# Kernel optimization log

Hardware: AMD Instinct MI355X
Metric: run time of the kernel (lower is better)

The kernel has to match this reference:

```python
import jax, jax.numpy as jnp
import numpy as np

B, S, D = 64, 8192, 128  # batch, source length, hidden (enc == dec)


def setup_inputs() -> dict:
    key = jax.random.key(0)
    ks = jax.random.split(key, 7)
    s = 1.0 / np.sqrt(D)
    return {
        "input": jax.random.normal(ks[0], (B, D), jnp.float32),
        "context": jax.random.normal(ks[1], (B, S, D), jnp.float32),
        "W_enc": jax.random.uniform(ks[2], (D, D), jnp.float32, -s, s),
        "b_enc": jax.random.uniform(ks[3], (D,), jnp.float32, -s, s),
        "W_dec": jax.random.uniform(ks[4], (D, D), jnp.float32, -s, s),
        "b_dec": jax.random.uniform(ks[5], (D,), jnp.float32, -s, s),
        "W_out": jax.random.uniform(ks[6], (D, 2 * D), jnp.float32, -s, s),  # no bias
    }


def reference(input, context, W_enc, b_enc, W_dec, b_dec, W_out):
    # projected_context = tanh(lin_encoder(context))  [B, S, D]
    pc = jnp.tanh(jnp.einsum("bse,de->bsd", context, W_enc) + b_enc)
    # q = tanh(lin_decoder(input))  [B, D]
    q = jnp.tanh(input @ W_dec.T + b_dec)
    # attention scores via bmm(projected_context, q): [B, S]
    scores = jnp.einsum("bsd,bd->bs", pc, q)
    attn = jax.nn.softmax(scores, axis=1)  # softmax over source positions
    # weighted sum of (raw) context: [B, D]
    weighted_context = jnp.einsum("bs,bsd->bd", attn, context)
    # h_tilde = tanh(linear_out(concat(weighted_context, q)))  [B, D]
    h_tilde = jnp.tanh(jnp.concatenate([weighted_context, q], axis=-1) @ W_out.T)
    return h_tilde, attn
```

## Files before the change

### kernel.cpp

```cpp
#include <hip/hip_runtime.h>
#include <hip/hip_bf16.h>

#define BB 64
#define SS 8192
#define DD 128
#define NCHUNK 8
#define CHROWS 1024
#define NTILE 16

typedef __attribute__((ext_vector_type(8))) short bf16x8;
typedef __attribute__((ext_vector_type(4))) float f32x4;

#define SWZ(c, qd) ((qd) * 16 + ((c) ^ (2 * (qd))))

__device__ __forceinline__ unsigned pk2(float x, float y) {
    __hip_bfloat162 h = __float22bfloat162_rn(make_float2(x, y));
    union { __hip_bfloat162 h2; unsigned u; } cv;
    cv.h2 = h;
    return cv.u;
}

__device__ __forceinline__ float bflo(unsigned p) { return __uint_as_float(p << 16); }
__device__ __forceinline__ float bfhi(unsigned p) { return __uint_as_float(p & 0xffff0000u); }

__device__ __forceinline__ float tanh_fast(float x) {
    float e = __expf(2.f * x);
    return 1.f - 2.f / (e + 1.f);
}

__device__ __forceinline__ void lds_barrier() {
    asm volatile("s_waitcnt lgkmcnt(0)" ::: "memory");
    __builtin_amdgcn_s_barrier();
    asm volatile("" ::: "memory");
}

__global__ void qproj_kernel(const float* __restrict__ input,
                             const float* __restrict__ W_dec,
                             const float* __restrict__ b_dec,
                             float* __restrict__ q) {
    __shared__ float xin[DD];
    const int b = blockIdx.x, d = threadIdx.x;
    xin[d] = input[b * DD + d];
    __syncthreads();
    const float4* wrow = (const float4*)(W_dec + (size_t)d * DD);
    float acc = 0.f;
#pragma unroll
    for (int k4 = 0; k4 < DD / 4; k4++) {
        float4 w = wrow[k4];
        float4 x = ((const float4*)xin)[k4];
        acc += w.x * x.x + w.y * x.y + w.z * x.z + w.w * x.w;
    }
    q[b * DD + d] = tanh_fast(acc + b_dec[d]);
}

#define ISSUE(tile, R) do {                                          \
    const float4* tb_ = base + (size_t)(tile) * 2048;                \
    _Pragma("unroll")                                                \
    for (int i = 0; i < 8; i++) R[i] = tb_[t + 256 * i];             \
} while (0)

#define PACK(buf, R) do {                                            \
    _Pragma("unroll")                                                \
    for (int i = 0; i < 8; i++) {                                    \
        int row_ = rg + 8 * i, w_ = row_ >> 4, c_ = row_ & 15;       \
        int a8_ = (w_ * 4 + ukk) * 128 + SWZ(c_, uqd) * 2 + uh;      \
        uint2 pk_;                                                   \
        pk_.x = pk2(R[i].x, R[i].y);                                 \
        pk_.y = pk2(R[i].z, R[i].w);                                 \
        P[i] = pk_;                                                  \
        *(uint2*)&Cl[buf][a8_ * 4] = pk_;                            \
    }                                                                \
} while (0)

__global__ __launch_bounds__(256, 2) void score_fused_kernel(
    const float* __restrict__ ctx,
    const float* __restrict__ W_enc,
    const float* __restrict__ b_enc,
    const float* __restrict__ q,
    float* __restrict__ scores,
    float* __restrict__ wcp,
    float* __restrict__ Mp,
    float* __restrict__ Tp) {
    __shared__ __align__(16) short Wl[16384];
    __shared__ __align__(16) short Cl[2][8192];
    __shared__ float sw[64];
    __shared__ float4 red[256];

    const int t = threadIdx.x;

    const float4* W4 = (const float4*)W_enc;
    for (int c2 = t; c2 < 2048; c2 += 256) {
        int row = c2 >> 4, kc = c2 & 15;
        float4 f0 = W4[row * 32 + kc * 2];
        float4 f1 = W4[row * 32 + kc * 2 + 1];
        int nt = row >> 4, colw = row & 15, kk = kc >> 2, qd = kc & 3;
        int a8 = (nt * 4 + kk) * 128 + SWZ(colw, qd) * 2;
        uint4 u;
        u.x = pk2(f0.x, f0.y); u.y = pk2(f0.z, f0.w);
        u.z = pk2(f1.x, f1.y); u.w = pk2(f1.z, f1.w);
        *(uint4*)&Wl[a8 * 4] = u;
    }

    const int wv = t >> 6, lane = t & 63;
    const int col = lane & 15, quad = lane >> 4;
    const int b = blockIdx.x >> 3;
    const int chunk = blockIdx.x & 7;

    const int u = t & 31, rg = t >> 5;
    const int ukk = u >> 3, uqd = (u >> 1) & 3, uh = u & 1;

    float qv[8], bv[8];
#pragma unroll
    for (int nt = 0; nt < 8; nt++) {
        qv[nt] = q[b * DD + nt * 16 + col];
        bv[nt] = b_enc[nt * 16 + col];
    }

    const float4* base = (const float4*)(ctx + ((size_t)b * SS + (size_t)chunk * CHROWS) * DD);

    float4 RA[8], RB[8];
    uint2 P[8];

    float Mrun = -INFINITY, Trun = 0.f;
    float4 acc4 = {0.f, 0.f, 0.f, 0.f};

    auto compute_tile = [&](int it, int cur) {
        bf16x8 a[4];
#pragma unroll
        for (int kk = 0; kk < 4; kk++) {
            int a8 = (wv * 4 + kk) * 128 + SWZ(col, quad) * 2;
            a[kk] = *(const bf16x8*)&Cl[cur][a8 * 4];
        }
        f32x4 acc[8];
#pragma unroll
        for (int nt = 0; nt < 8; nt++) {
            f32x4 c = {0.f, 0.f, 0.f, 0.f};
#pragma unroll
            for (int kk = 0; kk < 4; kk++) {
                int a8 = (nt * 4 + kk) * 128 + SWZ(col, quad) * 2;
                bf16x8 bf = *(const bf16x8*)&Wl[a8 * 4];
                c = __builtin_amdgcn_mfma_f32_16x16x32_bf16(a[kk], bf, c, 0, 0, 0);
            }
            acc[nt] = c;
        }
#pragma unroll
        for (int r = 0; r < 4; r++) {
            float v = 0.f;
#pragma unroll
            for (int nt = 0; nt < 8; nt++)
                v += tanh_fast(acc[nt][r] + bv[nt]) * qv[nt];
            v += __shfl_xor(v, 1);
            v += __shfl_xor(v, 2);
            v += __shfl_xor(v, 4);
            v += __shfl_xor(v, 8);
            if (col == 0) {
                int lrow = wv * 16 + quad * 4 + r;
                sw[lrow] = v;
                scores[(size_t)b * SS + (size_t)chunk * CHROWS + it * 64 + lrow] = v;
            }
        }
    };

    auto softmax_wsum = [&]() {
        float sv = sw[lane];
        float m = sv;
#pragma unroll
        for (int off = 1; off < 64; off <<= 1) m = fmaxf(m, __shfl_xor(m, off));
        float Mnew = fmaxf(Mrun, m);
        float alpha = __expf(Mrun - Mnew);
        float wlane = __expf(sv - Mnew);
        float ts = wlane;
#pragma unroll
        for (int off = 1; off < 64; off <<= 1) ts += __shfl_xor(ts, off);
        Trun = Trun * alpha + ts;
        Mrun = Mnew;

        acc4.x *= alpha; acc4.y *= alpha; acc4.z *= alpha; acc4.w *= alpha;
#pragma unroll
        for (int i = 0; i < 8; i++) {
            int row = rg + 8 * i;
            uint2 pk = P[i];
            float wi = __shfl(wlane, row);
            acc4.x += wi * bflo(pk.x);
            acc4.y += wi * bfhi(pk.x);
            acc4.z += wi * bflo(pk.y);
            acc4.w += wi * bfhi(pk.y);
        }
    };

    ISSUE(0, RA);
    ISSUE(1, RB);
    PACK(0, RA);
    lds_barrier();

    for (int it2 = 0; it2 < NTILE / 2; ++it2) {
        const int T = 2 * it2;

        if (T + 2 < NTILE) ISSUE(T + 2, RA);
        compute_tile(T, 0);
        lds_barrier();
        softmax_wsum();
        PACK(1, RB);
        lds_barrier();

        if (T + 3 < NTILE) ISSUE(T + 3, RB);
        compute_tile(T + 1, 1);
        lds_barrier();
        softmax_wsum();
        if (T + 2 < NTILE) PACK(0, RA);
        lds_barrier();
    }

    red[t] = acc4;
    __syncthreads();
    if (t < 32) {
        float4 s = red[t];
#pragma unroll
        for (int k = 1; k < 8; k++) {
            float4 p = red[t + 32 * k];
            s.x += p.x; s.y += p.y; s.z += p.z; s.w += p.w;
        }
        *(float4*)&wcp[(size_t)blockIdx.x * DD + 4 * t] = s;
    }
    if (t == 0) {
        Mp[blockIdx.x] = Mrun;
        Tp[blockIdx.x] = Trun;
    }
}

__global__ void combine_out_kernel(const float* __restrict__ wcp,
                                   const float* __restrict__ Mp,
                                   const float* __restrict__ Tp,
                                   const float* __restrict__ q,
                                   const float* __restrict__ W_out,
                                   float* __restrict__ h,
                                   float* __restrict__ Ms,
                                   float* __restrict__ Tinv) {
    __shared__ float cat[2 * DD];
    const int b = blockIdx.x, d = threadIdx.x;
    float M = -INFINITY;
#pragma unroll
    for (int j = 0; j < NCHUNK; j++) M = fmaxf(M, Mp[b * NCHUNK + j]);
    float T = 0.f, acc = 0.f;
#pragma unroll
    for (int j = 0; j < NCHUNK; j++) {
        float e = __expf(Mp[b * NCHUNK + j] - M);
        T += Tp[b * NCHUNK + j] * e;
        acc += wcp[(size_t)(b * NCHUNK + j) * DD + d] * e;
    }
    float ti = 1.f / T;
    cat[d] = acc * ti;
    cat[DD + d] = q[b * DD + d];
    if (d == 0) { Ms[b] = M; Tinv[b] = ti; }
    __syncthreads();
    const float4* wrow = (const float4*)(W_out + (size_t)d * 2 * DD);
    float a2 = 0.f;
#pragma unroll
    for (int k4 = 0; k4 < 2 * DD / 4; k4++) {
        float4 w = wrow[k4];
        float4 x = ((const float4*)cat)[k4];
        a2 += w.x * x.x + w.y * x.y + w.z * x.z + w.w * x.w;
    }
    h[b * DD + d] = tanh_fast(a2);
}

__global__ __launch_bounds__(512) void attnfin_kernel(const float* __restrict__ scores,
                                                      const float* __restrict__ Ms,
                                                      const float* __restrict__ Tinv,
                                                      float* __restrict__ attn) {
    const int b = blockIdx.x >> 2, seg = blockIdx.x & 3;
    const float M = Ms[b], ti = Tinv[b];
    const float4* s4 = (const float4*)(scores + (size_t)b * SS) + seg * 512;
    float4* a4 = (float4*)(attn + (size_t)b * SS) + seg * 512;
    float4 v = s4[threadIdx.x];
    v.x = __expf(v.x - M) * ti;
    v.y = __expf(v.y - M) * ti;
    v.z = __expf(v.z - M) * ti;
    v.w = __expf(v.w - M) * ti;
    a4[threadIdx.x] = v;
}

extern "C" void kernel_launch(void* const* d_in, const int* in_sizes, int n_in,
                              void* d_out, int out_size, void* d_ws, size_t ws_size,
                              hipStream_t stream) {
    const float* input = (const float*)d_in[0];
    const float* ctx   = (const float*)d_in[1];
    const float* W_enc = (const float*)d_in[2];
    const float* b_enc = (const float*)d_in[3];
    const float* W_dec = (const float*)d_in[4];
    const float* b_dec = (const float*)d_in[5];
    const float* W_out = (const float*)d_in[6];

    float* h    = (float*)d_out;
    float* attn = (float*)d_out + BB * DD;

    float* ws     = (float*)d_ws;
    float* q      = ws;
    float* scores = ws + 8192;
    float* wcp    = scores + 524288;
    float* Mp     = wcp + 512 * DD;
    float* Tp     = Mp + 512;
    float* Ms     = Tp + 512;
    float* Tinv   = Ms + 64;

    qproj_kernel<<<BB, DD, 0, stream>>>(input, W_dec, b_dec, q);
    score_fused_kernel<<<BB * NCHUNK, 256, 0, stream>>>(ctx, W_enc, b_enc, q,
                                                        scores, wcp, Mp, Tp);
    combine_out_kernel<<<BB, DD, 0, stream>>>(wcp, Mp, Tp, q, W_out, h, Ms, Tinv);
    attnfin_kernel<<<BB * 4, 512, 0, stream>>>(scores, Ms, Tinv, attn);
}
```

Measured before the change: 419.6 us.

## Restructure tile pipeline to one barrier per tile with double-buffered scores

The main loop now packs the next tile into LDS during the current tile's compute phase. The score scratch buffer is double-buffered, so each tile needs one LDS barrier instead of two. The two in-flight global load register sets are merged into one, with two packed-bf16 sets kept for the weighted-sum pass. This is meant to cut barrier stalls and register pressure. The cost is a shorter prefetch distance, one tile ahead instead of two, which may expose more global-load latency.

Measured after the change: 398.9 us. 4.9% less time.

```diff
diff --git a/kernel.cpp b/kernel.cpp
--- a/kernel.cpp
+++ b/kernel.cpp
@@ -52,25 +52,6 @@
     }
     q[b * DD + d] = tanh_fast(acc + b_dec[d]);
 }
-
-#define ISSUE(tile, R) do {                                          \
-    const float4* tb_ = base + (size_t)(tile) * 2048;                \
-    _Pragma("unroll")                                                \
-    for (int i = 0; i < 8; i++) R[i] = tb_[t + 256 * i];             \
-} while (0)
-
-#define PACK(buf, R) do {                                            \
-    _Pragma("unroll")                                                \
-    for (int i = 0; i < 8; i++) {                                    \
-        int row_ = rg + 8 * i, w_ = row_ >> 4, c_ = row_ & 15;       \
-        int a8_ = (w_ * 4 + ukk) * 128 + SWZ(c_, uqd) * 2 + uh;      \
-        uint2 pk_;                                                   \
-        pk_.x = pk2(R[i].x, R[i].y);                                 \
-        pk_.y = pk2(R[i].z, R[i].w);                                 \
-        P[i] = pk_;                                                  \
-        *(uint2*)&Cl[buf][a8_ * 4] = pk_;                            \
-    }                                                                \
-} while (0)
 
 __global__ __launch_bounds__(256, 2) void score_fused_kernel(
     const float* __restrict__ ctx,
@@ -83,7 +64,7 @@
     float* __restrict__ Tp) {
     __shared__ __align__(16) short Wl[16384];
     __shared__ __align__(16) short Cl[2][8192];
-    __shared__ float sw[64];
+    __shared__ float sw[2][64];
     __shared__ float4 red[256];
 
     const int t = threadIdx.x;
@@ -118,97 +99,111 @@
 
     const float4* base = (const float4*)(ctx + ((size_t)b * SS + (size_t)chunk * CHROWS) * DD);
 
-    float4 RA[8], RB[8];
-    uint2 P[8];
-
+    float4 R[8];
+    uint2 PA[8], PB[8];
     float Mrun = -INFINITY, Trun = 0.f;
     float4 acc4 = {0.f, 0.f, 0.f, 0.f};
 
-    auto compute_tile = [&](int it, int cur) {
-        bf16x8 a[4];
-#pragma unroll
-        for (int kk = 0; kk < 4; kk++) {
-            int a8 = (wv * 4 + kk) * 128 + SWZ(col, quad) * 2;
-            a[kk] = *(const bf16x8*)&Cl[cur][a8 * 4];
-        }
-        f32x4 acc[8];
-#pragma unroll
-        for (int nt = 0; nt < 8; nt++) {
-            f32x4 c = {0.f, 0.f, 0.f, 0.f};
-#pragma unroll
-            for (int kk = 0; kk < 4; kk++) {
-                int a8 = (nt * 4 + kk) * 128 + SWZ(col, quad) * 2;
-                bf16x8 bf = *(const bf16x8*)&Wl[a8 * 4];
-                c = __builtin_amdgcn_mfma_f32_16x16x32_bf16(a[kk], bf, c, 0, 0, 0);
-            }
-            acc[nt] = c;
-        }
-#pragma unroll
-        for (int r = 0; r < 4; r++) {
-            float v = 0.f;
-#pragma unroll
-            for (int nt = 0; nt < 8; nt++)
-                v += tanh_fast(acc[nt][r] + bv[nt]) * qv[nt];
-            v += __shfl_xor(v, 1);
-            v += __shfl_xor(v, 2);
-            v += __shfl_xor(v, 4);
-            v += __shfl_xor(v, 8);
-            if (col == 0) {
-                int lrow = wv * 16 + quad * 4 + r;
-                sw[lrow] = v;
-                scores[(size_t)b * SS + (size_t)chunk * CHROWS + it * 64 + lrow] = v;
-            }
-        }
-    };
-
-    auto softmax_wsum = [&]() {
-        float sv = sw[lane];
-        float m = sv;
-#pragma unroll
-        for (int off = 1; off < 64; off <<= 1) m = fmaxf(m, __shfl_xor(m, off));
-        float Mnew = fmaxf(Mrun, m);
-        float alpha = __expf(Mrun - Mnew);
-        float wlane = __expf(sv - Mnew);
-        float ts = wlane;
-#pragma unroll
-        for (int off = 1; off < 64; off <<= 1) ts += __shfl_xor(ts, off);
-        Trun = Trun * alpha + ts;
-        Mrun = Mnew;
-
-        acc4.x *= alpha; acc4.y *= alpha; acc4.z *= alpha; acc4.w *= alpha;
-#pragma unroll
-        for (int i = 0; i < 8; i++) {
-            int row = rg + 8 * i;
-            uint2 pk = P[i];
-            float wi = __shfl(wlane, row);
-            acc4.x += wi * bflo(pk.x);
-            acc4.y += wi * bfhi(pk.x);
-            acc4.z += wi * bflo(pk.y);
-            acc4.w += wi * bfhi(pk.y);
-        }
-    };
-
-    ISSUE(0, RA);
-    ISSUE(1, RB);
-    PACK(0, RA);
-    lds_barrier();
+#define ISSUE(tile) do {                                             \
+    const float4* tb_ = base + (size_t)(tile) * 2048;                \
+    _Pragma("unroll")                                                \
+    for (int i = 0; i < 8; i++) R[i] = tb_[t + 256 * i];             \
+} while (0)
+
+#define PACK(buf, P) do {                                            \
+    _Pragma("unroll")                                                \
+    for (int i = 0; i < 8; i++) {                                    \
+        int row_ = rg + 8 * i, w_ = row_ >> 4, c_ = row_ & 15;       \
+        int a8_ = (w_ * 4 + ukk) * 128 + SWZ(c_, uqd) * 2 + uh;      \
+        uint2 pk_;                                                   \
+        pk_.x = pk2(R[i].x, R[i].y);                                 \
+        pk_.y = pk2(R[i].z, R[i].w);                                 \
+        P[i] = pk_;                                                  \
+        *(uint2*)&Cl[buf][a8_ * 4] = pk_;                            \
+    }                                                                \
+} while (0)
+
+#define COMPUTE(it, cur, swb) do {                                   \
+    bf16x8 a_[4];                                                    \
+    _Pragma("unroll")                                                \
+    for (int kk = 0; kk < 4; kk++) {                                 \
+        int a8_ = (wv * 4 + kk) * 128 + SWZ(col, quad) * 2;          \
+        a_[kk] = *(const bf16x8*)&Cl[cur][a8_ * 4];                  \
+    }                                                                \
+    f32x4 acc_[8];                                                   \
+    _Pragma("unroll")                                                \
+    for (int nt = 0; nt < 8; nt++) {                                 \
+        f32x4 c_ = {0.f, 0.f, 0.f, 0.f};                             \
+        _Pragma("unroll")                                            \
+        for (int kk = 0; kk < 4; kk++) {                             \
+            int a8_ = (nt * 4 + kk) * 128 + SWZ(col, quad) * 2;      \
+            bf16x8 bf_ = *(const bf16x8*)&Wl[a8_ * 4];               \
+            c_ = __builtin_amdgcn_mfma_f32_16x16x32_bf16(a_[kk], bf_, c_, 0, 0, 0); \
+        }                                                            \
+        acc_[nt] = c_;                                               \
+    }                                                                \
+    _Pragma("unroll")                                                \
+    for (int r = 0; r < 4; r++) {                                    \
+        float v_ = 0.f;                                              \
+        _Pragma("unroll")                                            \
+        for (int nt = 0; nt < 8; nt++)                               \
+            v_ += tanh_fast(acc_[nt][r] + bv[nt]) * qv[nt];          \
+        v_ += __shfl_xor(v_, 1);                                     \
+        v_ += __shfl_xor(v_, 2);                                     \
+        v_ += __shfl_xor(v_, 4);                                     \
+        v_ += __shfl_xor(v_, 8);                                     \
+        if (col == 0) {                                              \
+            int lrow_ = wv * 16 + quad * 4 + r;                      \
+            sw[swb][lrow_] = v_;                                     \
+            scores[(size_t)b * SS + (size_t)chunk * CHROWS + (it) * 64 + lrow_] = v_; \
+        }                                                            \
+    }                                                                \
+} while (0)
+
+#define SMWSUM(P, swb) do {                                          \
+    float sv_ = sw[swb][lane];                                       \
+    float m_ = sv_;                                                  \
+    _Pragma("unroll")                                                \
+    for (int off = 1; off < 64; off <<= 1) m_ = fmaxf(m_, __shfl_xor(m_, off)); \
+    float Mn_ = fmaxf(Mrun, m_);                                     \
+    float al_ = __expf(Mrun - Mn_);                                  \
+    float wl_ = __expf(sv_ - Mn_);                                   \
+    float ts_ = wl_;                                                 \
+    _Pragma("unroll")                                                \
+    for (int off = 1; off < 64; off <<= 1) ts_ += __shfl_xor(ts_, off); \
+    Trun = Trun * al_ + ts_;                                         \
+    Mrun = Mn_;                                                      \
+    acc4.x *= al_; acc4.y *= al_; acc4.z *= al_; acc4.w *= al_;      \
+    _Pragma("unroll")                                                \
+    for (int i = 0; i < 8; i++) {                                    \
+        int row_ = rg + 8 * i;                                       \
+        uint2 pk_ = P[i];                                            \
+        float wi_ = __shfl(wl_, row_);                               \
+        acc4.x += wi_ * bflo(pk_.x);                                 \
+        acc4.y += wi_ * bfhi(pk_.x);                                 \
+        acc4.z += wi_ * bflo(pk_.y);                                 \
+        acc4.w += wi_ * bfhi(pk_.y);                                 \
+    }                                                                \
+} while (0)
+
+    ISSUE(0);
+    PACK(0, PA);
+    __syncthreads();
 
     for (int it2 = 0; it2 < NTILE / 2; ++it2) {
         const int T = 2 * it2;
 
-        if (T + 2 < NTILE) ISSUE(T + 2, RA);
-        compute_tile(T, 0);
+        ISSUE(T + 1);
+        COMPUTE(T, 0, 0);
+        PACK(1, PB);
         lds_barrier();
-        softmax_wsum();
-        PACK(1, RB);
+        SMWSUM(PA, 0);
+
+        if (T + 2 < NTILE) ISSUE(T + 2);
+        COMPUTE(T + 1, 1, 1);
+        if (T + 2 < NTILE) PACK(0, PA);
         lds_barrier();
-
-        if (T + 3 < NTILE) ISSUE(T + 3, RB);
-        compute_tile(T + 1, 1);
-        lds_barrier();
-        softmax_wsum();
-        if (T + 2 < NTILE) PACK(0, RA);
-        lds_barrier();
+        SMWSUM(PB, 1);
     }
 
     red[t] = acc4;
```
